# Kernel optimization log

Measured on AMD Instinct MI355X. Metric: run time of the kernel, lower is better.

## Reference

```python
import jax, jax.numpy as jnp
import numpy as np

N_NODES = 100000
N_EDGES = 3200000
IN_F, HID, N_CLS = 512, 16, 7


def setup_inputs() -> dict:
    key = jax.random.key(0)
    k1, k2, k3, k4 = jax.random.split(key, 4)
    x = jax.random.normal(k1, (N_NODES, IN_F), dtype=jnp.float32)
    edge_index = jax.random.randint(k2, (2, N_EDGES), 0, N_NODES, dtype=jnp.int32)
    W1 = jax.random.normal(k3, (IN_F, HID), dtype=jnp.float32) * (1.0 / np.sqrt(IN_F))
    b1 = jnp.zeros((HID,), dtype=jnp.float32)
    W2 = jax.random.normal(k4, (HID, N_CLS), dtype=jnp.float32) * (1.0 / np.sqrt(HID))
    b2 = jnp.zeros((N_CLS,), dtype=jnp.float32)
    return {"x": x, "edge_index": edge_index, "W1": W1, "b1": b1, "W2": W2, "b2": b2}


def _gcn_norm(src, dst, n_nodes):
    # symmetric normalization with self-loops already included in (src, dst)
    deg = jax.ops.segment_sum(jnp.ones(dst.shape, jnp.float32), dst, num_segments=n_nodes)
    dinv = jnp.where(deg > 0, jax.lax.rsqrt(deg), 0.0)
    return dinv[src] * dinv[dst]  # [E]


def _gcn_conv(h, src, dst, norm, W, b, n_nodes):
    # transform-first (PyG GCNConv), then normalized scatter-add aggregation
    h = h @ W                                   # [N, out]
    msg = h[src] * norm[:, None]                # gather + scale, [E, out]
    out = jax.ops.segment_sum(msg, dst, num_segments=n_nodes)  # scatter-add
    return out + b


def reference(x, edge_index, W1, b1, W2, b2):
    n = x.shape[0]
    loops = jnp.arange(n, dtype=edge_index.dtype)
    src = jnp.concatenate([edge_index[0], loops])
    dst = jnp.concatenate([edge_index[1], loops])
    norm = _gcn_norm(src, dst, n)
    h = _gcn_conv(x, src, dst, norm, W1, b1, n)
    h = jax.nn.relu(h)
    out = _gcn_conv(h, src, dst, norm, W2, b2, n)
    return out
```

## Files before the change

### kernel.cpp

```cpp
#include <hip/hip_runtime.h>

#define CHUNK 8192
#define BMAX 512

typedef __attribute__((address_space(3))) unsigned int lds_u32;
typedef const __attribute__((address_space(1))) unsigned int glb_u32;

__device__ __forceinline__ void gload16(const float* g, float* l) {
    __builtin_amdgcn_global_load_lds((glb_u32*)g, (lds_u32*)l, 16, 0, 0);
}


__global__ __launch_bounds__(256) void k_coarse_hist(const int* __restrict__ dst, int E,
                                                     int* __restrict__ bc,
                                                     int* __restrict__ blockBase, int B) {
    __shared__ int cnt[BMAX];
    int t = threadIdx.x;
    cnt[t] = 0; cnt[t + 256] = 0;
    __syncthreads();
    int e0 = blockIdx.x * CHUNK;
#pragma unroll
    for (int it = 0; it < CHUNK / 256; ++it) {
        int e = e0 + it * 256 + t;
        if (e < E) atomicAdd(&cnt[dst[e] >> 8], 1);
    }
    __syncthreads();
    for (int b = t; b < B; b += 256) {
        int c = cnt[b];
        if (c > 0) blockBase[(size_t)blockIdx.x * B + b] = atomicAdd(&bc[b], c);
    }
}

__global__ void k_scan_bsums(int* bsums, int nb) {
    __shared__ int s[2][512];
    int t = threadIdx.x;
    int v = (t < nb) ? bsums[t] : 0;
    int p = 0;
    s[0][t] = v;
    __syncthreads();
    for (int off = 1; off < 512; off <<= 1) {
        s[p ^ 1][t] = s[p][t] + ((t >= off) ? s[p][t - off] : 0);
        p ^= 1;
        __syncthreads();
    }
    if (t < nb) bsums[t] = s[p][t] - v;
}


__global__ __launch_bounds__(256) void k_coarse_scatter(const int* __restrict__ src,
                                                        const int* __restrict__ dst, int E,
                                                        const int* __restrict__ bucketBase,
                                                        const int* __restrict__ blockBase, int B,
                                                        unsigned int* __restrict__ ebuf) {
    __shared__ int run[BMAX];
    int t = threadIdx.x;
    run[t] = 0; run[t + 256] = 0;
    __syncthreads();
    int e0 = blockIdx.x * CHUNK;
#pragma unroll
    for (int it = 0; it < CHUNK / 256; ++it) {
        int e = e0 + it * 256 + t;
        if (e < E) {
            int d = dst[e];
            int b = d >> 8;
            int rank = atomicAdd(&run[b], 1);
            int pos = bucketBase[b] + blockBase[(size_t)blockIdx.x * B + b] + rank;
            ebuf[pos] = ((unsigned int)(d & 255) << 24) | (unsigned int)src[e];
        }
    }
}


__global__ __launch_bounds__(256) void k_bucket_hist(const unsigned int* __restrict__ ebuf,
                                                     const int* __restrict__ bucketBase,
                                                     int E, int N, int B,
                                                     int* __restrict__ hist,
                                                     float* __restrict__ dinv) {
    __shared__ int cnt[256];
    int t = threadIdx.x;
    int b = blockIdx.x;
    cnt[t] = 0;
    __syncthreads();
    int e0 = bucketBase[b];
    int e1 = (b + 1 < B) ? bucketBase[b + 1] : E;
    for (int e = e0 + t; e < e1; e += 256) atomicAdd(&cnt[ebuf[e] >> 24], 1);
    __syncthreads();
    int node = b * 256 + t;
    if (node < N) {
        hist[node] = cnt[t];
        dinv[node] = rsqrtf((float)(cnt[t] + 1));
    }
}


__global__ __launch_bounds__(256) void k_fine_scatter(const unsigned int* __restrict__ ebuf,
                                                      const int* __restrict__ bucketBase,
                                                      const int* __restrict__ hist,
                                                      int E, int N, int B,
                                                      int* __restrict__ rowStart,
                                                      int* __restrict__ csr_src) {
    __shared__ int s[2][256];
    __shared__ int cnt[256];
    int t = threadIdx.x;
    int b = blockIdx.x;
    int node = b * 256 + t;
    int v = (node < N) ? hist[node] : 0;
    int p = 0;
    s[0][t] = v;
    __syncthreads();
    for (int off = 1; off < 256; off <<= 1) {
        s[p ^ 1][t] = s[p][t] + ((t >= off) ? s[p][t - off] : 0);
        p ^= 1;
        __syncthreads();
    }
    int rs = bucketBase[b] + s[p][t] - v;
    if (node < N) rowStart[node] = rs;
    cnt[t] = rs;
    __syncthreads();
    int e0 = bucketBase[b];
    int e1 = (b + 1 < B) ? bucketBase[b + 1] : E;
    for (int e = e0 + t; e < e1; e += 256) {
        unsigned int w = ebuf[e];
        int pos = atomicAdd(&cnt[w >> 24], 1);
        csr_src[pos] = (int)(w & 0xFFFFFFu);
    }
}


__global__ __launch_bounds__(256) void k_gemm1(const float* __restrict__ x,
                                               const float* __restrict__ W1,
                                               const float* __restrict__ dinv,
                                               int N, float* __restrict__ h1) {
    __shared__ float xs[2][256 * 32];
    const int t = threadIdx.x;
    const int R0 = blockIdx.x * 256;
    const int tk = t & 7;

    const float* gbase[8];
#pragma unroll
    for (int it = 0; it < 8; ++it) {
        int r = it * 32 + (t >> 3);
        int j4 = tk ^ (r & 7);
        int row = R0 + r;
        if (row >= N) row = N - 1;
        gbase[it] = x + (size_t)row * 512 + j4 * 4;
    }

    float acc[16];
#pragma unroll
    for (int c = 0; c < 16; ++c) acc[c] = 0.0f;

#pragma unroll
    for (int it = 0; it < 8; ++it)
        gload16(gbase[it], &xs[0][(it * 256 + t) * 4]);
    __syncthreads();

    int p = 0;
    for (int ch = 0; ch < 16; ++ch) {
        if (ch + 1 < 16) {
#pragma unroll
            for (int it = 0; it < 8; ++it)
                gload16(gbase[it] + (ch + 1) * 32, &xs[p ^ 1][(it * 256 + t) * 4]);
        }
        const float* xr = &xs[p][t * 32];
#pragma unroll
        for (int j4 = 0; j4 < 8; ++j4) {
            float4 xv = *(const float4*)(xr + ((j4 ^ tk) << 2));
            float xe[4] = {xv.x, xv.y, xv.z, xv.w};
            int k = ch * 32 + j4 * 4;
#pragma unroll
            for (int d = 0; d < 4; ++d) {
                const float* w = W1 + (k + d) * 16;
#pragma unroll
                for (int c = 0; c < 16; ++c) acc[c] = fmaf(xe[d], w[c], acc[c]);
            }
        }
        __syncthreads();
        p ^= 1;
    }

    int row = R0 + t;
    if (row < N) {
        float di = dinv[row];
#pragma unroll
        for (int c = 0; c < 16; ++c) acc[c] *= di;
        float4* o = (float4*)(h1 + (size_t)row * 16);
        o[0] = make_float4(acc[0], acc[1], acc[2], acc[3]);
        o[1] = make_float4(acc[4], acc[5], acc[6], acc[7]);
        o[2] = make_float4(acc[8], acc[9], acc[10], acc[11]);
        o[3] = make_float4(acc[12], acc[13], acc[14], acc[15]);
    }
}


__global__ void k_gather1(const float* __restrict__ h1, const int* __restrict__ csr_src,
                          const int* __restrict__ rowStart, const int* __restrict__ hist,
                          const float* __restrict__ dinv, const float* __restrict__ b1,
                          int N, float* __restrict__ relu1) {
    int g = blockIdx.x * blockDim.x + threadIdx.x;
    int i = g >> 4, c = g & 15;
    if (i >= N) return;
    float ssum = h1[(size_t)i * 16 + c];
    int e0 = rowStart[i], e1 = e0 + hist[i];
    for (int e = e0; e < e1; ++e) {
        int s = csr_src[e];
        ssum += h1[(size_t)s * 16 + c];
    }
    float v = fmaf(dinv[i], ssum, b1[c]);
    relu1[(size_t)i * 16 + c] = fmaxf(v, 0.0f);
}


__global__ void k_h2(const float* __restrict__ relu1, const float* __restrict__ W2,
                     const float* __restrict__ dinv, int N, float* __restrict__ h2) {
    int i = blockIdx.x * blockDim.x + threadIdx.x;
    if (i >= N) return;
    float r[16];
#pragma unroll
    for (int q = 0; q < 4; ++q) {
        float4 v = *(const float4*)(relu1 + (size_t)i * 16 + q * 4);
        r[q * 4 + 0] = v.x; r[q * 4 + 1] = v.y; r[q * 4 + 2] = v.z; r[q * 4 + 3] = v.w;
    }
    float di = dinv[i];
#pragma unroll
    for (int c2 = 0; c2 < 7; ++c2) {
        float a = 0.0f;
#pragma unroll
        for (int c = 0; c < 16; ++c) a = fmaf(r[c], W2[c * 7 + c2], a);
        h2[(size_t)i * 7 + c2] = a * di;
    }
}


__global__ void k_gather2(const float* __restrict__ h2, const int* __restrict__ csr_src,
                          const int* __restrict__ rowStart, const int* __restrict__ hist,
                          const float* __restrict__ dinv, const float* __restrict__ b2,
                          int N, float* __restrict__ out) {
    int g = blockIdx.x * blockDim.x + threadIdx.x;
    int i = g >> 3, c = g & 7;
    if (i >= N || c >= 7) return;
    float ssum = h2[(size_t)i * 7 + c];
    int e0 = rowStart[i], e1 = e0 + hist[i];
    for (int e = e0; e < e1; ++e) {
        int s = csr_src[e];
        ssum += h2[(size_t)s * 7 + c];
    }
    out[(size_t)i * 7 + c] = fmaf(dinv[i], ssum, b2[c]);
}


extern "C" void kernel_launch(void* const* d_in, const int* in_sizes, int n_in,
                              void* d_out, int out_size, void* d_ws, size_t ws_size,
                              hipStream_t stream) {
    const float* x  = (const float*)d_in[0];
    const int*   ei = (const int*)d_in[1];
    const float* W1 = (const float*)d_in[2];
    const float* b1 = (const float*)d_in[3];
    const float* W2 = (const float*)d_in[4];
    const float* b2 = (const float*)d_in[5];
    float* out = (float*)d_out;

    const int N = in_sizes[0] / 512;
    const int E = in_sizes[1] / 2;
    const int* src = ei;
    const int* dst = ei + E;

    const int nb  = (N + 255) / 256;
    const int B   = nb;
    const int nbA = (E + CHUNK - 1) / CHUNK;

    char* ws = (char*)d_ws;
    auto alloc = [&](size_t bytes) {
        char* p = ws;
        ws += (bytes + 511) & ~(size_t)511;
        return p;
    };
    int*   hist      = (int*)alloc((size_t)N * 4);
    float* dinv      = (float*)alloc((size_t)N * 4);
    int*   rowStart  = (int*)alloc((size_t)N * 4);
    int*   bc        = (int*)alloc((size_t)(B + 1) * 4);
    int*   blockBase = (int*)alloc((size_t)nbA * B * 4);
    int*   csr_src   = (int*)alloc((size_t)E * 4);
    size_t featBytes = (size_t)N * 16 * 4 * 2 + (size_t)N * 7 * 4;
    size_t ebufBytes = (size_t)E * 4;
    char* regB = alloc(featBytes > ebufBytes ? featBytes : ebufBytes);
    unsigned int* ebuf = (unsigned int*)regB;
    float* h1    = (float*)regB;
    float* relu1 = h1 + (size_t)N * 16;
    float* h2    = relu1 + (size_t)N * 16;

    hipMemsetAsync(bc, 0, (size_t)B * 4, stream);
    k_coarse_hist<<<nbA, 256, 0, stream>>>(dst, E, bc, blockBase, B);
    k_scan_bsums<<<1, 512, 0, stream>>>(bc, B);
    k_coarse_scatter<<<nbA, 256, 0, stream>>>(src, dst, E, bc, blockBase, B, ebuf);
    k_bucket_hist<<<B, 256, 0, stream>>>(ebuf, bc, E, N, B, hist, dinv);
    k_fine_scatter<<<B, 256, 0, stream>>>(ebuf, bc, hist, E, N, B, rowStart, csr_src);
    k_gemm1<<<nb, 256, 0, stream>>>(x, W1, dinv, N, h1);
    k_gather1<<<(N * 16 + 255) / 256, 256, 0, stream>>>(h1, csr_src, rowStart, hist, dinv, b1, N, relu1);
    k_h2<<<nb, 256, 0, stream>>>(relu1, W2, dinv, N, h2);
    k_gather2<<<(N * 8 + 255) / 256, 256, 0, stream>>>(h2, csr_src, rowStart, hist, dinv, b2, N, out);
}
```

Baseline: 579.1 us.

## Rewrite GEMM1 as per-output-column threads with pre-permuted W1 layout

Replaces the LDS-staged, double-buffered GEMM (one row per thread, 16 accumulators) with a layout where 16 threads share one row, each computing one output column directly from global memory. A small pre-kernel permutes W1 so each thread reads its column weights as contiguous float4 vectors. The aim is more parallelism and fewer registers per thread. In exchange, each x row is read by 16 threads and the reads are no longer staged through LDS, so the code relies on the cache to coalesce the redundant loads.

```diff
diff --git a/kernel.cpp b/kernel.cpp
--- a/kernel.cpp
+++ b/kernel.cpp
@@ -2,13 +2,6 @@
 
 #define CHUNK 8192
 #define BMAX 512
-
-typedef __attribute__((address_space(3))) unsigned int lds_u32;
-typedef const __attribute__((address_space(1))) unsigned int glb_u32;
-
-__device__ __forceinline__ void gload16(const float* g, float* l) {
-    __builtin_amdgcn_global_load_lds((glb_u32*)g, (lds_u32*)l, 16, 0, 0);
-}
 
 
 __global__ __launch_bounds__(256) void k_coarse_hist(const int* __restrict__ dst, int E,
@@ -127,69 +120,44 @@
 }
 
 
+__global__ void k_prepW(const float* __restrict__ W1, float* __restrict__ Wb) {
+    int i = blockIdx.x * 256 + threadIdx.x;
+    if (i >= 8192) return;
+    int k = i >> 4, c = i & 15;
+    Wb[(k >> 5) * 512 + ((k >> 2) & 7) * 64 + c * 4 + (k & 3)] = W1[i];
+}
+
+
 __global__ __launch_bounds__(256) void k_gemm1(const float* __restrict__ x,
-                                               const float* __restrict__ W1,
+                                               const float* __restrict__ Wb,
                                                const float* __restrict__ dinv,
                                                int N, float* __restrict__ h1) {
-    __shared__ float xs[2][256 * 32];
     const int t = threadIdx.x;
-    const int R0 = blockIdx.x * 256;
-    const int tk = t & 7;
-
-    const float* gbase[8];
-#pragma unroll
-    for (int it = 0; it < 8; ++it) {
-        int r = it * 32 + (t >> 3);
-        int j4 = tk ^ (r & 7);
-        int row = R0 + r;
-        if (row >= N) row = N - 1;
-        gbase[it] = x + (size_t)row * 512 + j4 * 4;
-    }
-
-    float acc[16];
-#pragma unroll
-    for (int c = 0; c < 16; ++c) acc[c] = 0.0f;
-
-#pragma unroll
-    for (int it = 0; it < 8; ++it)
-        gload16(gbase[it], &xs[0][(it * 256 + t) * 4]);
-    __syncthreads();
-
-    int p = 0;
-    for (int ch = 0; ch < 16; ++ch) {
-        if (ch + 1 < 16) {
-#pragma unroll
-            for (int it = 0; it < 8; ++it)
-                gload16(gbase[it] + (ch + 1) * 32, &xs[p ^ 1][(it * 256 + t) * 4]);
+    const int c = t & 15;
+    const int row0 = blockIdx.x * 16 + (t >> 4);
+    const int row = (row0 < N) ? row0 : N - 1;
+    const float* xr = x + (size_t)row * 512;
+
+    float acc = 0.0f;
+    for (int kb = 0; kb < 16; ++kb) {
+        const float* xp = xr + kb * 32;
+        const float* wp = Wb + kb * 512 + c * 4;
+        float4 xv[8], wv[8];
+#pragma unroll
+        for (int j = 0; j < 8; ++j) {
+            xv[j] = *(const float4*)(xp + j * 4);
+            wv[j] = *(const float4*)(wp + j * 64);
         }
-        const float* xr = &xs[p][t * 32];
-#pragma unroll
-        for (int j4 = 0; j4 < 8; ++j4) {
-            float4 xv = *(const float4*)(xr + ((j4 ^ tk) << 2));
-            float xe[4] = {xv.x, xv.y, xv.z, xv.w};
-            int k = ch * 32 + j4 * 4;
-#pragma unroll
-            for (int d = 0; d < 4; ++d) {
-                const float* w = W1 + (k + d) * 16;
-#pragma unroll
-                for (int c = 0; c < 16; ++c) acc[c] = fmaf(xe[d], w[c], acc[c]);
-            }
+#pragma unroll
+        for (int j = 0; j < 8; ++j) {
+            acc = fmaf(xv[j].x, wv[j].x, acc);
+            acc = fmaf(xv[j].y, wv[j].y, acc);
+            acc = fmaf(xv[j].z, wv[j].z, acc);
+            acc = fmaf(xv[j].w, wv[j].w, acc);
         }
-        __syncthreads();
-        p ^= 1;
-    }
-
-    int row = R0 + t;
-    if (row < N) {
-        float di = dinv[row];
-#pragma unroll
-        for (int c = 0; c < 16; ++c) acc[c] *= di;
-        float4* o = (float4*)(h1 + (size_t)row * 16);
-        o[0] = make_float4(acc[0], acc[1], acc[2], acc[3]);
-        o[1] = make_float4(acc[4], acc[5], acc[6], acc[7]);
-        o[2] = make_float4(acc[8], acc[9], acc[10], acc[11]);
-        o[3] = make_float4(acc[12], acc[13], acc[14], acc[15]);
-    }
+    }
+
+    if (row0 < N) h1[(size_t)row0 * 16 + c] = acc * dinv[row0];
 }
 
 
@@ -268,6 +236,7 @@
     const int nb  = (N + 255) / 256;
     const int B   = nb;
     const int nbA = (E + CHUNK - 1) / CHUNK;
+    const int nbG = (N + 15) / 16;
 
     char* ws = (char*)d_ws;
     auto alloc = [&](size_t bytes) {
@@ -281,6 +250,7 @@
     int*   bc        = (int*)alloc((size_t)(B + 1) * 4);
     int*   blockBase = (int*)alloc((size_t)nbA * B * 4);
     int*   csr_src   = (int*)alloc((size_t)E * 4);
+    float* Wb        = (float*)alloc(8192 * 4);
     size_t featBytes = (size_t)N * 16 * 4 * 2 + (size_t)N * 7 * 4;
     size_t ebufBytes = (size_t)E * 4;
     char* regB = alloc(featBytes > ebufBytes ? featBytes : ebufBytes);
@@ -290,12 +260,13 @@
     float* h2    = relu1 + (size_t)N * 16;
 
     hipMemsetAsync(bc, 0, (size_t)B * 4, stream);
+    k_prepW<<<32, 256, 0, stream>>>(W1, Wb);
     k_coarse_hist<<<nbA, 256, 0, stream>>>(dst, E, bc, blockBase, B);
     k_scan_bsums<<<1, 512, 0, stream>>>(bc, B);
     k_coarse_scatter<<<nbA, 256, 0, stream>>>(src, dst, E, bc, blockBase, B, ebuf);
     k_bucket_hist<<<B, 256, 0, stream>>>(ebuf, bc, E, N, B, hist, dinv);
     k_fine_scatter<<<B, 256, 0, stream>>>(ebuf, bc, hist, E, N, B, rowStart, csr_src);
-    k_gemm1<<<nb, 256, 0, stream>>>(x, W1, dinv, N, h1);
+    k_gemm1<<<nbG, 256, 0, stream>>>(x, Wb, dinv, N, h1);
     k_gather1<<<(N * 16 + 255) / 256, 256, 0, stream>>>(h1, csr_src, rowStart, hist, dinv, b1, N, relu1);
     k_h2<<<nb, 256, 0, stream>>>(relu1, W2, dinv, N, h2);
     k_gather2<<<(N * 8 + 255) / 256, 256, 0, stream>>>(h2, csr_src, rowStart, hist, dinv, b2, N, out);
```

Result: slower. 711.5 us (+22.9%).
